# Performance work log

Measured on AMD Instinct MI355X. Metric: run time of the kernel, lower is better.

Reference implementation:

```python
import jax, jax.numpy as jnp
import numpy as np

N_NODES = 50000


def _gcn_conv(x, src, dst, W, b, n_nodes):
    # x: [N, Fin] -> h: [N, Fout]; GCN: D^-1/2 (A+I) D^-1/2 (x W) + b
    h = x @ W
    deg = jax.ops.segment_sum(jnp.ones_like(dst, dtype=h.dtype), dst,
                              num_segments=n_nodes)
    dinv = jax.lax.rsqrt(jnp.maximum(deg, 1.0))
    norm = dinv[src] * dinv[dst]                      # [E]
    msg = h[src] * norm[:, None]                      # [E, Fout] gather
    agg = jax.ops.segment_sum(msg, dst, num_segments=n_nodes)  # scatter-add
    return agg + b


def setup_inputs() -> dict:
    key = jax.random.key(0)
    k0, k1, k2, k3 = jax.random.split(key, 4)
    N, E, F_IN, H, C = N_NODES, 800000, 128, 128, 16
    x = jax.random.normal(k0, (N, F_IN), dtype=jnp.float32)
    edge_index = jax.random.randint(k1, (2, E), 0, N, dtype=jnp.int64)
    W1 = jax.random.normal(k2, (F_IN, H), dtype=jnp.float32) / np.sqrt(F_IN)
    b1 = jnp.zeros((H,), dtype=jnp.float32)
    W2 = jax.random.normal(k3, (H, C), dtype=jnp.float32) / np.sqrt(H)
    b2 = jnp.zeros((C,), dtype=jnp.float32)
    return {"x": x, "edge_index": edge_index, "W1": W1, "b1": b1,
            "W2": W2, "b2": b2}


def reference(x, edge_index, W1, b1, W2, b2):
    n = x.shape[0]
    # add self-loops (shared by both conv layers)
    loops = jnp.arange(n, dtype=edge_index.dtype)
    src = jnp.concatenate([edge_index[0], loops])
    dst = jnp.concatenate([edge_index[1], loops])
    h = _gcn_conv(x, src, dst, W1, b1, n)
    h = jax.nn.relu(h)
    # dropout p=0.5 is identity in eval mode
    h = _gcn_conv(h, src, dst, W2, b2, n)
    return jax.nn.log_softmax(h, axis=1)
```

## Files before the change

### kernel.cpp

```cpp
#include <hip/hip_runtime.h>
#include <hip/hip_fp16.h>
#include <math.h>


#define NBUCKET_SHIFT 8
#define BIN_CHUNK 4096
#define PAD_SLOP (15 << NBUCKET_SHIFT)
#define CAP  5120
#define CCAP (CAP + PAD_SLOP)

typedef __bf16 bf16x8 __attribute__((ext_vector_type(8)));
typedef float  f32x4  __attribute__((ext_vector_type(4)));
typedef float  f32x2  __attribute__((ext_vector_type(2)));

__device__ __forceinline__ unsigned short pack_bf16(float f) {
    unsigned u = __float_as_uint(f);
    return (unsigned short)((u + 0x7fffu + ((u >> 16) & 1u)) >> 16);
}

__device__ __forceinline__ void acc_fp8x16(f32x2* a, uint4 v) {
    a[0] += __builtin_amdgcn_cvt_pk_f32_fp8(v.x, false);
    a[1] += __builtin_amdgcn_cvt_pk_f32_fp8(v.x, true);
    a[2] += __builtin_amdgcn_cvt_pk_f32_fp8(v.y, false);
    a[3] += __builtin_amdgcn_cvt_pk_f32_fp8(v.y, true);
    a[4] += __builtin_amdgcn_cvt_pk_f32_fp8(v.z, false);
    a[5] += __builtin_amdgcn_cvt_pk_f32_fp8(v.z, true);
    a[6] += __builtin_amdgcn_cvt_pk_f32_fp8(v.w, false);
    a[7] += __builtin_amdgcn_cvt_pk_f32_fp8(v.w, true);
}

__device__ __forceinline__ void acc_fp16x8(f32x2* a, uint4 v) {
    float2 f;
    f = __half22float2(*(const __half2*)&v.x); a[0] += *(f32x2*)&f;
    f = __half22float2(*(const __half2*)&v.y); a[1] += *(f32x2*)&f;
    f = __half22float2(*(const __half2*)&v.z); a[2] += *(f32x2*)&f;
    f = __half22float2(*(const __half2*)&v.w); a[3] += *(f32x2*)&f;
}

__global__ __launch_bounds__(256)
void bin_wt_kernel(const int* __restrict__ src, const int* __restrict__ dst,
                   int* __restrict__ bcur, unsigned* __restrict__ pairs,
                   int E, int nbuckets, int nbins,
                   const float* __restrict__ W, unsigned short* __restrict__ wtp) {
    const int blk = blockIdx.x;
    const int tid = threadIdx.x;
    if (blk >= nbins) {
        int idx = (blk - nbins) * 256 + tid;
        int j    = idx & 7;
        int lane = (idx >> 3) & 63;
        int ks   = (idx >> 9) & 3;
        int t    = idx >> 11;
        int n = t * 16 + (lane & 15);
        int k = ks * 32 + ((lane >> 4) << 3) + j;
        wtp[idx] = pack_bf16(W[k * 128 + n]);
        return;
    }
    __shared__ unsigned spair[BIN_CHUNK];
    __shared__ int lcnt[256];
    __shared__ int lbase[256];
    const int e0 = blk * BIN_CHUNK;
    const int cnt = min(BIN_CHUNK, E - e0);

    lcnt[tid] = 0;
    __syncthreads();
    for (int i = tid; i < cnt; i += 256) {
        unsigned s = (unsigned)src[e0 + i], d = (unsigned)dst[e0 + i];
        spair[i] = (d >> NBUCKET_SHIFT) << 24 | (d & 255u) << 16 | s;
        atomicAdd(&lcnt[d >> NBUCKET_SHIFT], 1);
    }
    __syncthreads();

    if (tid < nbuckets) {
        int c = lcnt[tid];
        lbase[tid] = (c > 0) ? atomicAdd(&bcur[tid], c) : 0;
        lcnt[tid] = 0;
    }
    __syncthreads();

    for (int i = tid; i < cnt; i += 256) {
        unsigned p = spair[i];
        int b = (int)(p >> 24);
        int off = atomicAdd(&lcnt[b], 1);
        pairs[b * CAP + lbase[b] + off] = p;
    }
}

__global__ __launch_bounds__(256)
void bucket_build_kernel(const int* __restrict__ bcur, const unsigned* __restrict__ pairs,
                         int* __restrict__ rowptr, int* __restrict__ rowcnt,
                         float* __restrict__ dinv, int* __restrict__ colsrc,
                         unsigned* __restrict__ h1b, unsigned* __restrict__ h2u,
                         int N, int nbuckets) {
    __shared__ int cnt[256];
    __shared__ int sm[256];
    const int tid = threadIdx.x;
    const int blk = blockIdx.x;
    const int nb0 = blk << NBUCKET_SHIFT;

    if (blk == 0) {
        if (tid < 32) h1b[(size_t)N * 32 + tid] = 0u;
        else if (tid < 40) h2u[(size_t)N * 8 + (tid - 32)] = 0u;
    }

    const int lo = blk * CAP;
    const int hi = lo + bcur[blk];
    cnt[tid] = 0;
    __syncthreads();

    for (int i = lo + tid; i < hi; i += 256)
        atomicAdd(&cnt[(int)(pairs[i] >> 16) & 255], 1);
    __syncthreads();

    int v = cnt[tid];
    int pdeg = (v + 15) & ~15;
    sm[tid] = pdeg;
    __syncthreads();
#pragma unroll
    for (int off = 1; off < 256; off <<= 1) {
        int u = (tid >= off) ? sm[tid - off] : 0;
        __syncthreads();
        sm[tid] += u;
        __syncthreads();
    }
    int pexcl = sm[tid] - pdeg;
    const int start = blk * CCAP + pexcl;
    int node = nb0 + tid;
    if (node < N) {
        rowptr[node] = start;
        rowcnt[node] = pdeg;
        dinv[node] = rsqrtf((float)v + 1.0f);
    }
    __syncthreads();
    cnt[tid] = start;
    __syncthreads();
    for (int i = lo + tid; i < hi; i += 256) {
        unsigned p = pairs[i];
        int pos = atomicAdd(&cnt[(int)(p >> 16) & 255], 1);
        colsrc[pos] = (int)(p & 0xffffu);
    }
    for (int p = start + v; p < start + pdeg; ++p)
        colsrc[p] = N;
}

__global__ __launch_bounds__(256)
void gemm1_mfma_kernel(const float* __restrict__ x, const unsigned short* __restrict__ wtp,
                       const float* __restrict__ dinv, unsigned* __restrict__ h1b, int N) {
    __shared__ float lds[4][16 * 132];
    const int tid = threadIdx.x, wave = tid >> 6, lane = tid & 63;
    const int q = lane >> 4, m = lane & 15;
    const int row0 = blockIdx.x * 64 + wave * 16;
    const int row = row0 + m;
    const int rowc = (row < N) ? row : (N - 1);

    f32x4 acc[8];
#pragma unroll
    for (int t = 0; t < 8; t++) acc[t] = (f32x4)0.0f;

#pragma unroll
    for (int ks = 0; ks < 4; ks++) {
        const float4* xp = (const float4*)(x + (size_t)rowc * 128 + ks * 32 + q * 8);
        float4 f0 = xp[0], f1 = xp[1];
        float fv[8] = {f0.x, f0.y, f0.z, f0.w, f1.x, f1.y, f1.z, f1.w};
        bf16x8 ah, al;
#pragma unroll
        for (int j = 0; j < 8; j++) {
            __bf16 h = (__bf16)fv[j];
            ah[j] = h;
            al[j] = (__bf16)(fv[j] - (float)h);
        }
#pragma unroll
        for (int t = 0; t < 8; t++) {
            bf16x8 b = *(const bf16x8*)(wtp + (size_t)(t * 4 + ks) * 512 + lane * 8);
            acc[t] = __builtin_amdgcn_mfma_f32_16x16x32_bf16(ah, b, acc[t], 0, 0, 0);
            acc[t] = __builtin_amdgcn_mfma_f32_16x16x32_bf16(al, b, acc[t], 0, 0, 0);
        }
    }

#pragma unroll
    for (int t = 0; t < 8; t++)
#pragma unroll
        for (int r = 0; r < 4; r++)
            lds[wave][(q * 4 + r) * 132 + t * 16 + m] = acc[t][r];
    __syncthreads();

    const int r2 = lane >> 2, j = lane & 3;
    const int orow = row0 + r2;
    if (orow < N) {
        float dv = dinv[orow];
        const float* lrow = &lds[wave][r2 * 132];
#pragma unroll
        for (int s = 0; s < 4; s++) {
            float4 a = *(const float4*)(lrow + s * 32 + j * 8);
            float4 b = *(const float4*)(lrow + s * 32 + j * 8 + 4);
            unsigned lo = __builtin_amdgcn_cvt_pk_fp8_f32(a.x * dv, a.y * dv, 0, false);
            lo = __builtin_amdgcn_cvt_pk_fp8_f32(a.z * dv, a.w * dv, lo, true);
            unsigned hi = __builtin_amdgcn_cvt_pk_fp8_f32(b.x * dv, b.y * dv, 0, false);
            hi = __builtin_amdgcn_cvt_pk_fp8_f32(b.z * dv, b.w * dv, hi, true);
            ((uint2*)h1b)[(size_t)orow * 16 + s * 4 + j] = make_uint2(lo, hi);
        }
    }
}

__global__ __launch_bounds__(256)
void l1_fused_kernel(const int* __restrict__ rowptr, const int* __restrict__ rowcnt,
                     const int* __restrict__ colsrc,
                     const float* __restrict__ dinv, const unsigned* __restrict__ h1b,
                     const float* __restrict__ b1, const float* __restrict__ W2,
                     __half* __restrict__ h2s, int N) {
    __shared__ float rows[4][2][132];
    __shared__ float w2s[128 * 16];
    const int tid = threadIdx.x;
    const int wave = tid >> 6, lane = tid & 63;
    const int c = lane & 7;
    const int g = (lane >> 3) & 3;
    const int n = lane >> 5;
    const int d = blockIdx.x * 8 + wave * 2 + n;

    for (int i = tid; i < 512; i += 256)
        ((float4*)w2s)[i] = ((const float4*)W2)[i];

    const uint4* hq = (const uint4*)h1b;

    if (d < N) {
        f32x2 a[8];
#pragma unroll
        for (int j = 0; j < 8; j++) a[j] = (f32x2)0.0f;

        if (g == 0)
            acc_fp8x16(a, hq[(size_t)d * 8 + c]);

        int i = rowptr[d];
        const int end = i + rowcnt[d];
        int s0 = 0, s1 = 0, s2 = 0, s3 = 0;
        if (i < end) {
            s0 = colsrc[i + g];      s1 = colsrc[i + g + 4];
            s2 = colsrc[i + g + 8];  s3 = colsrc[i + g + 12];
        }
        while (i < end) {
            uint4 v0 = hq[(size_t)s0 * 8 + c];
            uint4 v1 = hq[(size_t)s1 * 8 + c];
            uint4 v2 = hq[(size_t)s2 * 8 + c];
            uint4 v3 = hq[(size_t)s3 * 8 + c];
            i += 16;
            if (i < end) {
                s0 = colsrc[i + g];      s1 = colsrc[i + g + 4];
                s2 = colsrc[i + g + 8];  s3 = colsrc[i + g + 12];
            }
            acc_fp8x16(a, v0); acc_fp8x16(a, v1);
            acc_fp8x16(a, v2); acc_fp8x16(a, v3);
        }

#pragma unroll
        for (int j = 0; j < 8; j++) {
            a[j].x += __shfl_xor(a[j].x, 8, 64);
            a[j].y += __shfl_xor(a[j].y, 8, 64);
            a[j].x += __shfl_xor(a[j].x, 16, 64);
            a[j].y += __shfl_xor(a[j].y, 16, 64);
        }

        if (g == 0) {
            float dv = dinv[d];
            float* rbase = &rows[wave][n][c * 16];
#pragma unroll
            for (int t = 0; t < 4; t++) {
                float4 bb = ((const float4*)b1)[c * 4 + t];
                float4 o;
                o.x = fmaxf(a[2 * t].x * dv + bb.x, 0.0f);
                o.y = fmaxf(a[2 * t].y * dv + bb.y, 0.0f);
                o.z = fmaxf(a[2 * t + 1].x * dv + bb.z, 0.0f);
                o.w = fmaxf(a[2 * t + 1].y * dv + bb.w, 0.0f);
                *(float4*)(rbase + 4 * t) = o;
            }
        }
    }
    __syncthreads();

    const int n2 = lane >> 5, kh = (lane >> 4) & 1, col = lane & 15;
    const int d2 = blockIdx.x * 8 + wave * 2 + n2;
    if (d2 < N) {
        const float* r = &rows[wave][n2][kh * 64];
        const float* w = &w2s[kh * 64 * 16];
        float p = 0.0f;
#pragma unroll
        for (int k = 0; k < 64; k++)
            p = fmaf(r[k], w[k * 16 + col], p);
        p += __shfl_xor(p, 16, 64);
        if (kh == 0)
            h2s[(size_t)d2 * 16 + col] = __float2half_rn(p * dinv[d2]);
    }
}

__global__ __launch_bounds__(256)
void l2_kernel(const int* __restrict__ rowptr, const int* __restrict__ rowcnt,
               const int* __restrict__ colsrc,
               const float* __restrict__ dinv, const unsigned* __restrict__ h2s,
               const float* __restrict__ b2, float* __restrict__ out, int N) {
    const int tid = threadIdx.x;
    const int wave = tid >> 6, lane = tid & 63;
    const int n = lane >> 5;
    const int g = (lane >> 1) & 15;
    const int c = lane & 1;
    const int d = blockIdx.x * 8 + wave * 2 + n;
    if (d >= N) return;
    const uint4* h2q = (const uint4*)h2s;

    f32x2 a[4];
#pragma unroll
    for (int j = 0; j < 4; j++) a[j] = (f32x2)0.0f;

    if (g == 0)
        acc_fp16x8(a, h2q[(size_t)d * 2 + c]);

    int i = rowptr[d];
    const int end = i + rowcnt[d];
    int s = (i < end) ? colsrc[i + g] : 0;
    while (i < end) {
        uint4 v = h2q[(size_t)s * 2 + c];
        i += 16;
        if (i < end) s = colsrc[i + g];
        acc_fp16x8(a, v);
    }

#pragma unroll
    for (int j = 0; j < 4; j++) {
#pragma unroll
        for (int off = 2; off <= 16; off <<= 1) {
            a[j].x += __shfl_xor(a[j].x, off, 64);
            a[j].y += __shfl_xor(a[j].y, off, 64);
        }
    }

    const float dv = dinv[d];
    const float* af = (const float*)a;
    float v8[8];
#pragma unroll
    for (int j = 0; j < 8; j++) v8[j] = af[j] * dv + b2[c * 8 + j];

    float m = v8[0];
#pragma unroll
    for (int j = 1; j < 8; j++) m = fmaxf(m, v8[j]);
    m = fmaxf(m, __shfl_xor(m, 1, 64));
    float e = 0.0f;
#pragma unroll
    for (int j = 0; j < 8; j++) e += expf(v8[j] - m);
    e += __shfl_xor(e, 1, 64);
    float lse = m + logf(e);

    if (g == 0) {
        float4 o0 = make_float4(v8[0] - lse, v8[1] - lse, v8[2] - lse, v8[3] - lse);
        float4 o1 = make_float4(v8[4] - lse, v8[5] - lse, v8[6] - lse, v8[7] - lse);
        float4* op = (float4*)(out + (size_t)d * 16 + c * 8);
        op[0] = o0; op[1] = o1;
    }
}

extern "C" void kernel_launch(void* const* d_in, const int* in_sizes, int n_in,
                              void* d_out, int out_size, void* d_ws, size_t ws_size,
                              hipStream_t stream) {
    const float* x  = (const float*)d_in[0];
    const int*  ei  = (const int*)d_in[1];
    const float* W1 = (const float*)d_in[2];
    const float* b1 = (const float*)d_in[3];
    const float* W2 = (const float*)d_in[4];
    const float* b2 = (const float*)d_in[5];
    float* out = (float*)d_out;

    const int N = in_sizes[0] / 128;
    const int E = in_sizes[1] / 2;
    const int* src = ei;
    const int* dst = ei + E;
    const int nbuckets = (N + 255) >> NBUCKET_SHIFT;
    const int nbins = (E + BIN_CHUNK - 1) / BIN_CHUNK;

    float*          wsf     = (float*)d_ws;
    float*          dinv    = wsf;
    int*            rowptr  = (int*)(wsf + N);
    int*            rowcnt  = rowptr + N;
    int*            bcur    = rowcnt + N;
    unsigned short* wtp     = (unsigned short*)(bcur + 256);
    int*            colsrc  = bcur + 256 + 8192;
    unsigned*       pairs   = (unsigned*)(colsrc + (size_t)nbuckets * CCAP);
    unsigned*       h1b     = pairs + (size_t)nbuckets * CAP;
    unsigned*       h2u     = h1b + (size_t)(N + 1) * 32;

    hipMemsetAsync(bcur, 0, 256 * sizeof(int), stream);
    bin_wt_kernel<<<nbins + 64, 256, 0, stream>>>(src, dst, bcur, pairs, E,
                                                  nbuckets, nbins, W1, wtp);
    bucket_build_kernel<<<nbuckets, 256, 0, stream>>>(bcur, pairs, rowptr, rowcnt,
                                                      dinv, colsrc, h1b, h2u,
                                                      N, nbuckets);

    gemm1_mfma_kernel<<<(N + 63) / 64, 256, 0, stream>>>(x, wtp, dinv, h1b, N);

    l1_fused_kernel<<<(N + 7) / 8, 256, 0, stream>>>(rowptr, rowcnt, colsrc, dinv,
                                                     h1b, b1, W2, (__half*)h2u, N);

    l2_kernel<<<(N + 7) / 8, 256, 0, stream>>>(rowptr, rowcnt, colsrc, dinv, h2u,
                                               b2, out, N);
}
```

Before: 167.4 us.

## Fuse layer-1 GEMM into edge-binning kernel and move source normalization into gather

The x@W1 MFMA GEMM now runs as extra blocks of the edge-binning kernel, so it no longer waits for degrees or runs as a separate launch. Each GEMM block converts W1 to the packed bf16 layout in shared memory, which drops the separate weight-prep blocks and their global buffer. Because dinv is not yet known when the GEMM runs, h1 is stored without source scaling, and the layer-1 aggregation instead loads dinv[src] per edge and multiplies during accumulation. A padded zero entry dinv[N] is added for the padding sentinel. The trade is an extra per-edge dinv gather and multiply in the hot aggregation loop, a W1 repack in every GEMM block, and FP8 storage of unscaled values, which shifts the quantisation range.

```diff
diff --git a/kernel.cpp b/kernel.cpp
--- a/kernel.cpp
+++ b/kernel.cpp
@@ -18,15 +18,16 @@
     return (unsigned short)((u + 0x7fffu + ((u >> 16) & 1u)) >> 16);
 }
 
-__device__ __forceinline__ void acc_fp8x16(f32x2* a, uint4 v) {
-    a[0] += __builtin_amdgcn_cvt_pk_f32_fp8(v.x, false);
-    a[1] += __builtin_amdgcn_cvt_pk_f32_fp8(v.x, true);
-    a[2] += __builtin_amdgcn_cvt_pk_f32_fp8(v.y, false);
-    a[3] += __builtin_amdgcn_cvt_pk_f32_fp8(v.y, true);
-    a[4] += __builtin_amdgcn_cvt_pk_f32_fp8(v.z, false);
-    a[5] += __builtin_amdgcn_cvt_pk_f32_fp8(v.z, true);
-    a[6] += __builtin_amdgcn_cvt_pk_f32_fp8(v.w, false);
-    a[7] += __builtin_amdgcn_cvt_pk_f32_fp8(v.w, true);
+__device__ __forceinline__ void acc_fp8x16_fma(f32x2* a, uint4 v, float w) {
+    f32x2 ww; ww.x = w; ww.y = w;
+    a[0] += __builtin_amdgcn_cvt_pk_f32_fp8(v.x, false) * ww;
+    a[1] += __builtin_amdgcn_cvt_pk_f32_fp8(v.x, true)  * ww;
+    a[2] += __builtin_amdgcn_cvt_pk_f32_fp8(v.y, false) * ww;
+    a[3] += __builtin_amdgcn_cvt_pk_f32_fp8(v.y, true)  * ww;
+    a[4] += __builtin_amdgcn_cvt_pk_f32_fp8(v.z, false) * ww;
+    a[5] += __builtin_amdgcn_cvt_pk_f32_fp8(v.z, true)  * ww;
+    a[6] += __builtin_amdgcn_cvt_pk_f32_fp8(v.w, false) * ww;
+    a[7] += __builtin_amdgcn_cvt_pk_f32_fp8(v.w, true)  * ww;
 }
 
 __device__ __forceinline__ void acc_fp16x8(f32x2* a, uint4 v) {
@@ -37,51 +38,111 @@
     f = __half22float2(*(const __half2*)&v.w); a[3] += *(f32x2*)&f;
 }
 
+union K1Smem {
+    struct { unsigned spair[BIN_CHUNK]; int lcnt[256]; int lbase[256]; } b;
+    unsigned short wtp[16384];
+    float outb[4][16 * 132];
+};
+
 __global__ __launch_bounds__(256)
-void bin_wt_kernel(const int* __restrict__ src, const int* __restrict__ dst,
-                   int* __restrict__ bcur, unsigned* __restrict__ pairs,
-                   int E, int nbuckets, int nbins,
-                   const float* __restrict__ W, unsigned short* __restrict__ wtp) {
+void bin_gemm1_kernel(const int* __restrict__ src, const int* __restrict__ dst,
+                      int* __restrict__ bcur, unsigned* __restrict__ pairs,
+                      int E, int nbuckets, int nbins,
+                      const float* __restrict__ x, const float* __restrict__ W1,
+                      unsigned* __restrict__ h1b, int N) {
+    __shared__ K1Smem sm;
     const int blk = blockIdx.x;
     const int tid = threadIdx.x;
-    if (blk >= nbins) {
-        int idx = (blk - nbins) * 256 + tid;
-        int j    = idx & 7;
-        int lane = (idx >> 3) & 63;
-        int ks   = (idx >> 9) & 3;
-        int t    = idx >> 11;
-        int n = t * 16 + (lane & 15);
-        int k = ks * 32 + ((lane >> 4) << 3) + j;
-        wtp[idx] = pack_bf16(W[k * 128 + n]);
+
+    if (blk < nbins) {
+        const int e0 = blk * BIN_CHUNK;
+        const int cnt = min(BIN_CHUNK, E - e0);
+        sm.b.lcnt[tid] = 0;
+        __syncthreads();
+        for (int i = tid; i < cnt; i += 256) {
+            unsigned s = (unsigned)src[e0 + i], d = (unsigned)dst[e0 + i];
+            sm.b.spair[i] = (d >> NBUCKET_SHIFT) << 24 | (d & 255u) << 16 | s;
+            atomicAdd(&sm.b.lcnt[d >> NBUCKET_SHIFT], 1);
+        }
+        __syncthreads();
+        if (tid < nbuckets) {
+            int c = sm.b.lcnt[tid];
+            sm.b.lbase[tid] = (c > 0) ? atomicAdd(&bcur[tid], c) : 0;
+            sm.b.lcnt[tid] = 0;
+        }
+        __syncthreads();
+        for (int i = tid; i < cnt; i += 256) {
+            unsigned p = sm.b.spair[i];
+            int b = (int)(p >> 24);
+            int off = atomicAdd(&sm.b.lcnt[b], 1);
+            pairs[b * CAP + sm.b.lbase[b] + off] = p;
+        }
         return;
     }
-    __shared__ unsigned spair[BIN_CHUNK];
-    __shared__ int lcnt[256];
-    __shared__ int lbase[256];
-    const int e0 = blk * BIN_CHUNK;
-    const int cnt = min(BIN_CHUNK, E - e0);
-
-    lcnt[tid] = 0;
-    __syncthreads();
-    for (int i = tid; i < cnt; i += 256) {
-        unsigned s = (unsigned)src[e0 + i], d = (unsigned)dst[e0 + i];
-        spair[i] = (d >> NBUCKET_SHIFT) << 24 | (d & 255u) << 16 | s;
-        atomicAdd(&lcnt[d >> NBUCKET_SHIFT], 1);
-    }
-    __syncthreads();
-
-    if (tid < nbuckets) {
-        int c = lcnt[tid];
-        lbase[tid] = (c > 0) ? atomicAdd(&bcur[tid], c) : 0;
-        lcnt[tid] = 0;
-    }
-    __syncthreads();
-
-    for (int i = tid; i < cnt; i += 256) {
-        unsigned p = spair[i];
-        int b = (int)(p >> 24);
-        int off = atomicAdd(&lcnt[b], 1);
-        pairs[b * CAP + lbase[b] + off] = p;
+
+    const int gblk = blk - nbins;
+    const int wave = tid >> 6, lane = tid & 63;
+    const int q = lane >> 4, m = lane & 15;
+    const int row0 = gblk * 64 + wave * 16;
+    const int row = row0 + m;
+    const int rowc = (row < N) ? row : (N - 1);
+
+    for (int it = tid; it < 16384; it += 256) {
+        int k = it >> 7, n = it & 127;
+        int t = n >> 4, mm = n & 15;
+        int ks = k >> 5;
+        int lane2 = (((k & 31) >> 3) << 4) | mm;
+        int j = k & 7;
+        sm.wtp[(t * 4 + ks) * 512 + lane2 * 8 + j] = pack_bf16(W1[it]);
+    }
+    __syncthreads();
+
+    f32x4 acc[8];
+#pragma unroll
+    for (int t = 0; t < 8; t++) acc[t] = (f32x4)0.0f;
+
+#pragma unroll
+    for (int ks = 0; ks < 4; ks++) {
+        const float4* xp = (const float4*)(x + (size_t)rowc * 128 + ks * 32 + q * 8);
+        float4 f0 = xp[0], f1 = xp[1];
+        float fv[8] = {f0.x, f0.y, f0.z, f0.w, f1.x, f1.y, f1.z, f1.w};
+        bf16x8 ah, al;
+#pragma unroll
+        for (int j = 0; j < 8; j++) {
+            __bf16 h = (__bf16)fv[j];
+            ah[j] = h;
+            al[j] = (__bf16)(fv[j] - (float)h);
+        }
+#pragma unroll
+        for (int t = 0; t < 8; t++) {
+            bf16x8 b = *(const bf16x8*)(sm.wtp + (size_t)(t * 4 + ks) * 512 + lane * 8);
+            acc[t] = __builtin_amdgcn_mfma_f32_16x16x32_bf16(ah, b, acc[t], 0, 0, 0);
+            acc[t] = __builtin_amdgcn_mfma_f32_16x16x32_bf16(al, b, acc[t], 0, 0, 0);
+        }
+    }
+    __syncthreads();
+
+#pragma unroll
+    for (int t = 0; t < 8; t++)
+#pragma unroll
+        for (int r = 0; r < 4; r++)
+            sm.outb[wave][(q * 4 + r) * 132 + t * 16 + m] = acc[t][r];
+    __syncthreads();
+
+    const int r2 = lane >> 2, j = lane & 3;
+    const int orow = row0 + r2;
+    if (orow < N) {
+        const float* lrow = &sm.outb[wave][r2 * 132];
+#pragma unroll
+        for (int s = 0; s < 4; s++) {
+            float4 a = *(const float4*)(lrow + s * 32 + j * 8);
+            float4 b = *(const float4*)(lrow + s * 32 + j * 8 + 4);
+            unsigned lo = __builtin_amdgcn_cvt_pk_fp8_f32(a.x, a.y, 0, false);
+            lo = __builtin_amdgcn_cvt_pk_fp8_f32(a.z, a.w, lo, true);
+            unsigned hi = __builtin_amdgcn_cvt_pk_fp8_f32(b.x, b.y, 0, false);
+            hi = __builtin_amdgcn_cvt_pk_fp8_f32(b.z, b.w, hi, true);
+            ((uint2*)h1b)[(size_t)orow * 16 + s * 4 + j] = make_uint2(lo, hi);
+        }
     }
 }
 
@@ -100,6 +161,7 @@
     if (blk == 0) {
         if (tid < 32) h1b[(size_t)N * 32 + tid] = 0u;
         else if (tid < 40) h2u[(size_t)N * 8 + (tid - 32)] = 0u;
+        else if (tid == 40) dinv[N] = 0.0f;
     }
 
     const int lo = blk * CAP;
@@ -140,65 +202,6 @@
     }
     for (int p = start + v; p < start + pdeg; ++p)
         colsrc[p] = N;
-}
-
-__global__ __launch_bounds__(256)
-void gemm1_mfma_kernel(const float* __restrict__ x, const unsigned short* __restrict__ wtp,
-                       const float* __restrict__ dinv, unsigned* __restrict__ h1b, int N) {
-    __shared__ float lds[4][16 * 132];
-    const int tid = threadIdx.x, wave = tid >> 6, lane = tid & 63;
-    const int q = lane >> 4, m = lane & 15;
-    const int row0 = blockIdx.x * 64 + wave * 16;
-    const int row = row0 + m;
-    const int rowc = (row < N) ? row : (N - 1);
-
-    f32x4 acc[8];
-#pragma unroll
-    for (int t = 0; t < 8; t++) acc[t] = (f32x4)0.0f;
-
-#pragma unroll
-    for (int ks = 0; ks < 4; ks++) {
-        const float4* xp = (const float4*)(x + (size_t)rowc * 128 + ks * 32 + q * 8);
-        float4 f0 = xp[0], f1 = xp[1];
-        float fv[8] = {f0.x, f0.y, f0.z, f0.w, f1.x, f1.y, f1.z, f1.w};
-        bf16x8 ah, al;
-#pragma unroll
-        for (int j = 0; j < 8; j++) {
-            __bf16 h = (__bf16)fv[j];
-            ah[j] = h;
-            al[j] = (__bf16)(fv[j] - (float)h);
-        }
-#pragma unroll
-        for (int t = 0; t < 8; t++) {
-            bf16x8 b = *(const bf16x8*)(wtp + (size_t)(t * 4 + ks) * 512 + lane * 8);
-            acc[t] = __builtin_amdgcn_mfma_f32_16x16x32_bf16(ah, b, acc[t], 0, 0, 0);
-            acc[t] = __builtin_amdgcn_mfma_f32_16x16x32_bf16(al, b, acc[t], 0, 0, 0);
-        }
-    }
-
-#pragma unroll
-    for (int t = 0; t < 8; t++)
-#pragma unroll
-        for (int r = 0; r < 4; r++)
-            lds[wave][(q * 4 + r) * 132 + t * 16 + m] = acc[t][r];
-    __syncthreads();
-
-    const int r2 = lane >> 2, j = lane & 3;
-    const int orow = row0 + r2;
-    if (orow < N) {
-        float dv = dinv[orow];
-        const float* lrow = &lds[wave][r2 * 132];
-#pragma unroll
-        for (int s = 0; s < 4; s++) {
-            float4 a = *(const float4*)(lrow + s * 32 + j * 8);
-            float4 b = *(const float4*)(lrow + s * 32 + j * 8 + 4);
-            unsigned lo = __builtin_amdgcn_cvt_pk_fp8_f32(a.x * dv, a.y * dv, 0, false);
-            lo = __builtin_amdgcn_cvt_pk_fp8_f32(a.z * dv, a.w * dv, lo, true);
-            unsigned hi = __builtin_amdgcn_cvt_pk_fp8_f32(b.x * dv, b.y * dv, 0, false);
-            hi = __builtin_amdgcn_cvt_pk_fp8_f32(b.z * dv, b.w * dv, hi, true);
-            ((uint2*)h1b)[(size_t)orow * 16 + s * 4 + j] = make_uint2(lo, hi);
-        }
-    }
 }
 
 __global__ __launch_bounds__(256)
@@ -222,12 +225,13 @@
     const uint4* hq = (const uint4*)h1b;
 
     if (d < N) {
+        const float dvd = dinv[d];
         f32x2 a[8];
 #pragma unroll
         for (int j = 0; j < 8; j++) a[j] = (f32x2)0.0f;
 
         if (g == 0)
-            acc_fp8x16(a, hq[(size_t)d * 8 + c]);
+            acc_fp8x16_fma(a, hq[(size_t)d * 8 + c], dvd);
 
         int i = rowptr[d];
         const int end = i + rowcnt[d];
@@ -241,13 +245,14 @@
             uint4 v1 = hq[(size_t)s1 * 8 + c];
             uint4 v2 = hq[(size_t)s2 * 8 + c];
             uint4 v3 = hq[(size_t)s3 * 8 + c];
+            float w0 = dinv[s0], w1 = dinv[s1], w2 = dinv[s2], w3 = dinv[s3];
             i += 16;
             if (i < end) {
                 s0 = colsrc[i + g];      s1 = colsrc[i + g + 4];
                 s2 = colsrc[i + g + 8];  s3 = colsrc[i + g + 12];
             }
-            acc_fp8x16(a, v0); acc_fp8x16(a, v1);
-            acc_fp8x16(a, v2); acc_fp8x16(a, v3);
+            acc_fp8x16_fma(a, v0, w0); acc_fp8x16_fma(a, v1, w1);
+            acc_fp8x16_fma(a, v2, w2); acc_fp8x16_fma(a, v3, w3);
         }
 
 #pragma unroll
@@ -259,16 +264,15 @@
         }
 
         if (g == 0) {
-            float dv = dinv[d];
             float* rbase = &rows[wave][n][c * 16];
 #pragma unroll
             for (int t = 0; t < 4; t++) {
                 float4 bb = ((const float4*)b1)[c * 4 + t];
                 float4 o;
-                o.x = fmaxf(a[2 * t].x * dv + bb.x, 0.0f);
-                o.y = fmaxf(a[2 * t].y * dv + bb.y, 0.0f);
-                o.z = fmaxf(a[2 * t + 1].x * dv + bb.z, 0.0f);
-                o.w = fmaxf(a[2 * t + 1].y * dv + bb.w, 0.0f);
+                o.x = fmaxf(a[2 * t].x * dvd + bb.x, 0.0f);
+                o.y = fmaxf(a[2 * t].y * dvd + bb.y, 0.0f);
+                o.z = fmaxf(a[2 * t + 1].x * dvd + bb.z, 0.0f);
+                o.w = fmaxf(a[2 * t + 1].y * dvd + bb.w, 0.0f);
                 *(float4*)(rbase + 4 * t) = o;
             }
         }
@@ -371,27 +375,27 @@
     const int* dst = ei + E;
     const int nbuckets = (N + 255) >> NBUCKET_SHIFT;
     const int nbins = (E + BIN_CHUNK - 1) / BIN_CHUNK;
+    const int g1blocks = (N + 63) / 64;
 
     float*          wsf     = (float*)d_ws;
     float*          dinv    = wsf;
-    int*            rowptr  = (int*)(wsf + N);
+    int*            rowptr  = (int*)(wsf + N + 16);
     int*            rowcnt  = rowptr + N;
     int*            bcur    = rowcnt + N;
-    unsigned short* wtp     = (unsigned short*)(bcur + 256);
-    int*            colsrc  = bcur + 256 + 8192;
+    int*            colsrc  = bcur + 256;
     unsigned*       pairs   = (unsigned*)(colsrc + (size_t)nbuckets * CCAP);
     unsigned*       h1b     = pairs + (size_t)nbuckets * CAP;
     unsigned*       h2u     = h1b + (size_t)(N + 1) * 32;
 
     hipMemsetAsync(bcur, 0, 256 * sizeof(int), stream);
-    bin_wt_kernel<<<nbins + 64, 256, 0, stream>>>(src, dst, bcur, pairs, E,
-                                                  nbuckets, nbins, W1, wtp);
+    bin_gemm1_kernel<<<nbins + g1blocks, 256, 0, stream>>>(src, dst, bcur, pairs,
+                                                           E, nbuckets, nbins,
+                                                           x, W1, h1b, N);
+
     bucket_build_kernel<<<nbuckets, 256, 0, stream>>>(bcur, pairs, rowptr, rowcnt,
                                                       dinv, colsrc, h1b, h2u,
                                                       N, nbuckets);
 
-    gemm1_mfma_kernel<<<(N + 63) / 64, 256, 0, stream>>>(x, wtp, dinv, h1b, N);
-
     l1_fused_kernel<<<(N + 7) / 8, 256, 0, stream>>>(rowptr, rowcnt, colsrc, dinv,
                                                      h1b, b1, W2, (__half*)h2u, N);
 
```

Measured after the change: 162.0 us. 3.2% less time.
